# Performance work log

Hardware: AMD Instinct MI355X
Metric: run time of the kernel (lower is better)

The kernel has to match this reference:

```python
import jax, jax.numpy as jnp
import numpy as np

H = 5120       # hidden_size
NH = 128       # num_heads
QLR = 1536     # q_lora_rank
DR = 64        # qk_rope_head_dim
KVLR = 512     # kv_lora_rank
DV = 128       # v_head_dim
DN = 128       # qk_nope_head_dim
DQ = 192       # q_head_dim
THETA = 10000.0
EPS = 1e-6


def _rmsnorm(x, w, eps=EPS):
    xf = x.astype(jnp.float32)
    var = jnp.mean(xf * xf, axis=-1, keepdims=True)
    return (w * (xf * jax.lax.rsqrt(var + eps))).astype(x.dtype)


def _rope(x, cos, sin):
    # Llama-style complex rotation on interleaved pairs along last dim.
    xr = x.reshape(x.shape[:-1] + (-1, 2))
    x0, x1 = xr[..., 0], xr[..., 1]
    out = jnp.stack([x0 * cos - x1 * sin, x0 * sin + x1 * cos], axis=-1)
    return out.reshape(x.shape)


def setup_inputs() -> dict:
    key = jax.random.key(0)
    ks = jax.random.split(key, 8)
    b, kv_len = 2, 2048
    s = 0.02  # scaled-down normal init for numerical sanity (math unchanged)
    return {
        "hidden_states": jax.random.normal(ks[0], (b, 1, H), jnp.float32),
        "compressed_kv_normed_cache": jax.random.normal(ks[1], (b, kv_len, KVLR), jnp.float32),
        "k_pe_cache": jax.random.normal(ks[2], (b, kv_len, DR), jnp.float32),
        "q_a_w": jax.random.normal(ks[3], (QLR, H), jnp.float32) * s,
        "q_a_ln_w": jnp.ones((QLR,), jnp.float32),
        "q_b_w": jax.random.normal(ks[4], (NH * DQ, QLR), jnp.float32) * s,
        "kv_b_w": jax.random.normal(ks[5], (NH * (DN + DV), KVLR), jnp.float32) * s,
        "o_w": jax.random.normal(ks[6], (H, NH * DV), jnp.float32) * s,
    }


def reference(hidden_states, compressed_kv_normed_cache, k_pe_cache,
              q_a_w, q_a_ln_w, q_b_w, kv_b_w, o_w):
    b = hidden_states.shape[0]
    kv_len = k_pe_cache.shape[1]

    # Q path: down-proj -> RMSNorm -> up-proj
    q_a = jnp.einsum('bqh,rh->bqr', hidden_states, q_a_w)          # [b,1,QLR]
    q_a = _rmsnorm(q_a, q_a_ln_w)
    q = jnp.einsum('bqr,or->bqo', q_a, q_b_w).reshape(b, NH, DQ)   # q_len==1
    q_nope, q_pe = q[..., :DN], q[..., DN:]                        # [b,NH,128],[b,NH,64]

    # RoPE tables
    inv_freq = 1.0 / (THETA ** (jnp.arange(0, DR, 2, dtype=jnp.float32) / DR))  # [32]
    ang = jnp.arange(kv_len, dtype=jnp.float32)[:, None] * inv_freq             # [kv_len,32]
    cos, sin = jnp.cos(ang), jnp.sin(ang)

    # query rotated at position kv_len-1 (torch code repeats q then takes last slot)
    q_pe = _rope(q_pe, cos[-1], sin[-1])                           # [b,NH,64]
    k_pe = _rope(k_pe_cache, cos[None], sin[None])                 # [b,kv_len,64]

    # KV decompression (shared latent -> per-head nope-key and value)
    kv = jnp.einsum('bkc,oc->bko', compressed_kv_normed_cache, kv_b_w)
    kv = kv.reshape(b, kv_len, NH, DN + DV)
    k_nope, v = kv[..., :DN], kv[..., DN:]                         # [b,kv,NH,128] each

    # scores: nope part + rope part (k_pe broadcast across heads)
    scores = (jnp.einsum('bhd,bkhd->bhk', q_nope, k_nope)
              + jnp.einsum('bhd,bkd->bhk', q_pe, k_pe)) * (DQ ** -0.5)
    attn = jax.nn.softmax(scores.astype(jnp.float32), axis=-1).astype(hidden_states.dtype)

    out = jnp.einsum('bhk,bkhd->bhd', attn, v).reshape(b, 1, NH * DV)
    return jnp.einsum('bqo,ho->bqh', out, o_w)                     # [b,1,H]
```

## Files before the change

### kernel.cpp

```cpp
#include <hip/hip_runtime.h>
#include <math.h>

constexpr int kH    = 5120;
constexpr int kQLR  = 1536;
constexpr int kNH   = 128;
constexpr int kDQ   = 192;
constexpr int kDN   = 128;
constexpr int kDR   = 64;
constexpr int kKVLR = 512;
constexpr int kDV   = 128;

template<int IN, int SPLIT, bool ATOMIC>
__global__ __launch_bounds__(256) void gemv2_k(const float* __restrict__ W,
                                               const float* __restrict__ x,
                                               float* __restrict__ y, int R) {
  constexpr int CH = IN / SPLIT;
  constexpr int F4 = CH / 256;
  int lane = threadIdx.x & 63, wave = threadIdx.x >> 6;
  int r0 = blockIdx.x * 8 + wave * 2;
  int c0 = blockIdx.y * CH;
  const float4* W0 = (const float4*)(W + (size_t)r0 * IN + c0);
  const float4* W1 = (const float4*)(W + (size_t)(r0 + 1) * IN + c0);
  const float4* x0 = (const float4*)(x + c0);
  const float4* x1 = (const float4*)(x + IN + c0);
  float a00 = 0.f, a01 = 0.f, a10 = 0.f, a11 = 0.f;
#pragma unroll 4
  for (int i = 0; i < F4; ++i) {
    int idx = lane + (i << 6);
    float4 w0 = W0[idx];
    float4 w1 = W1[idx];
    float4 u = x0[idx];
    float4 v = x1[idx];
    a00 = fmaf(w0.x,u.x,fmaf(w0.y,u.y,fmaf(w0.z,u.z,fmaf(w0.w,u.w,a00))));
    a01 = fmaf(w0.x,v.x,fmaf(w0.y,v.y,fmaf(w0.z,v.z,fmaf(w0.w,v.w,a01))));
    a10 = fmaf(w1.x,u.x,fmaf(w1.y,u.y,fmaf(w1.z,u.z,fmaf(w1.w,u.w,a10))));
    a11 = fmaf(w1.x,v.x,fmaf(w1.y,v.y,fmaf(w1.z,v.z,fmaf(w1.w,v.w,a11))));
  }
#pragma unroll
  for (int off = 32; off > 0; off >>= 1) {
    a00 += __shfl_down(a00, off, 64);
    a01 += __shfl_down(a01, off, 64);
    a10 += __shfl_down(a10, off, 64);
    a11 += __shfl_down(a11, off, 64);
  }
  if (lane == 0) {
    if (ATOMIC) {
      atomicAdd(&y[r0], a00);
      atomicAdd(&y[(size_t)R + r0], a01);
      atomicAdd(&y[r0 + 1], a10);
      atomicAdd(&y[(size_t)R + r0 + 1], a11);
    } else {
      y[r0] = a00;
      y[(size_t)R + r0] = a01;
      y[r0 + 1] = a10;
      y[(size_t)R + r0 + 1] = a11;
    }
  }
}

__global__ __launch_bounds__(256) void rmsnorm_k(const float* __restrict__ qa,
                                                 const float* __restrict__ w,
                                                 float* __restrict__ out) {
  int b = blockIdx.x, t = threadIdx.x;
  const float* x = qa + (size_t)b * kQLR;
  float s = 0.f;
  for (int i = t; i < kQLR; i += 256) { float v = x[i]; s = fmaf(v, v, s); }
  __shared__ float red[4];
#pragma unroll
  for (int off = 32; off > 0; off >>= 1) s += __shfl_down(s, off, 64);
  if ((t & 63) == 0) red[t >> 6] = s;
  __syncthreads();
  float tot = red[0] + red[1] + red[2] + red[3];
  float scale = rsqrtf(tot / (float)kQLR + 1e-6f);
  for (int i = t; i < kQLR; i += 256) out[(size_t)b * kQLR + i] = x[i] * scale * w[i];
}

__global__ __launch_bounds__(256) void rope_q_k(float* __restrict__ q, int pos) {
  int p = blockIdx.x * 256 + threadIdx.x;
  int i = p & 31;
  int h = (p >> 5) & (kNH - 1);
  int b = p >> 12;
  float inv = powf(10000.0f, -(float)i * (1.0f / 32.0f));
  float ang = (float)pos * inv;
  float s, c;
  sincosf(ang, &s, &c);
  float* base = q + ((size_t)b * kNH + h) * kDQ + kDN + 2 * i;
  float x0 = base[0], x1 = base[1];
  base[0] = x0 * c - x1 * s;
  base[1] = x0 * s + x1 * c;
}

__global__ __launch_bounds__(256) void rope_k_k(const float* __restrict__ kin,
                                                float* __restrict__ kout, int KV) {
  int p = blockIdx.x * 256 + threadIdx.x;
  int i = p & 31;
  int bk = p >> 5;
  int b = bk / KV;
  int k = bk - b * KV;
  float inv = powf(10000.0f, -(float)i * (1.0f / 32.0f));
  float ang = (float)k * inv;
  float s, c;
  sincosf(ang, &s, &c);
  const float* src = kin + ((size_t)b * KV + k) * kDR + 2 * i;
  float* dst = kout + ((size_t)b * KV + k) * kDR + 2 * i;
  float x0 = src[0], x1 = src[1];
  dst[0] = x0 * c - x1 * s;
  dst[1] = x0 * s + x1 * c;
}

__global__ __launch_bounds__(256) void qabs_k(const float* __restrict__ q,
                                              const float* __restrict__ kvw,
                                              float* __restrict__ qabs) {
  int h = blockIdx.x, ds = blockIdx.y;
  int t = threadIdx.x;
  __shared__ float qn[2][32];
  if (t < 64) {
    int b = t >> 5, d = t & 31;
    qn[b][d] = q[((size_t)b * kNH + h) * kDQ + ds * 32 + d];
  }
  __syncthreads();
  float a0x = 0.f, a0y = 0.f, a1x = 0.f, a1y = 0.f;
  const float* wb = kvw + ((size_t)h * 256 + ds * 32) * kKVLR + t * 2;
#pragma unroll 4
  for (int d = 0; d < 32; ++d) {
    float2 w = *(const float2*)(wb + (size_t)d * kKVLR);
    float q0 = qn[0][d], q1 = qn[1][d];
    a0x = fmaf(q0, w.x, a0x); a0y = fmaf(q0, w.y, a0y);
    a1x = fmaf(q1, w.x, a1x); a1y = fmaf(q1, w.y, a1y);
  }
  float* p0 = qabs + (size_t)h * kKVLR + t * 2;
  float* p1 = qabs + ((size_t)kNH + h) * kKVLR + t * 2;
  atomicAdd(p0, a0x); atomicAdd(p0 + 1, a0y);
  atomicAdd(p1, a1x); atomicAdd(p1 + 1, a1y);
}

__global__ __launch_bounds__(256) void scores_k(const float* __restrict__ qabs,
                                                const float* __restrict__ qfull,
                                                const float* __restrict__ c,
                                                const float* __restrict__ kper,
                                                float* __restrict__ scores, int KV) {
  int kc = blockIdx.x, hg = blockIdx.y, b = blockIdx.z;
  int t = threadIdx.x, lane = t & 63, wave = t >> 6;
  int h0 = __builtin_amdgcn_readfirstlane(hg * 16 + wave * 4);
  int k0 = kc * 64;
  __shared__ float cl[64 * 129];
  __shared__ float kl[64 * 65];
  float acc[4] = {0.f, 0.f, 0.f, 0.f};

  {
    const float4* src = (const float4*)(kper + ((size_t)b * KV + k0) * kDR);
#pragma unroll
    for (int i = 0; i < 4; ++i) {
      int idx = t + i * 256;
      int r = idx >> 4, c4 = idx & 15;
      float4 v = src[r * 16 + c4];
      float* d = &kl[r * 65 + (c4 << 2)];
      d[0] = v.x; d[1] = v.y; d[2] = v.z; d[3] = v.w;
    }
  }

  for (int cch = 0; cch < 4; ++cch) {
    __syncthreads();
    const float* cb = c + ((size_t)b * KV + k0) * kKVLR + cch * 128;
#pragma unroll
    for (int i = 0; i < 8; ++i) {
      int idx = t + i * 256;
      int r = idx >> 5, c4 = idx & 31;
      float4 v = *(const float4*)(cb + (size_t)r * kKVLR + (c4 << 2));
      float* d = &cl[r * 129 + (c4 << 2)];
      d[0] = v.x; d[1] = v.y; d[2] = v.z; d[3] = v.w;
    }
    __syncthreads();
    const float* qb = qabs + ((size_t)b * kNH + h0) * kKVLR + cch * 128;
#pragma unroll 4
    for (int cc = 0; cc < 128; ++cc) {
      float cv = cl[lane * 129 + cc];
#pragma unroll
      for (int j = 0; j < 4; ++j)
        acc[j] = fmaf(cv, qb[(size_t)j * kKVLR + cc], acc[j]);
    }
  }

  {
    const float* qp = qfull + ((size_t)b * kNH + h0) * kDQ + kDN;
#pragma unroll 4
    for (int i = 0; i < 64; ++i) {
      float kv = kl[lane * 65 + i];
#pragma unroll
      for (int j = 0; j < 4; ++j)
        acc[j] = fmaf(kv, qp[j * kDQ + i], acc[j]);
    }
  }

  const float scale = 1.0f / sqrtf(192.0f);
#pragma unroll
  for (int j = 0; j < 4; ++j)
    scores[((size_t)b * kNH + h0 + j) * KV + k0 + lane] = acc[j] * scale;
}

__global__ __launch_bounds__(256) void softmax_k(float* __restrict__ sc, int KV) {
  int t = threadIdx.x;
  float* row = sc + (size_t)blockIdx.x * KV;
  float vals[8];
  float m = -1e30f;
#pragma unroll
  for (int i = 0; i < 8; ++i) {
    vals[i] = row[t + i * 256];
    m = fmaxf(m, vals[i]);
  }
  __shared__ float red[4];
#pragma unroll
  for (int off = 32; off > 0; off >>= 1) m = fmaxf(m, __shfl_down(m, off, 64));
  if ((t & 63) == 0) red[t >> 6] = m;
  __syncthreads();
  m = fmaxf(fmaxf(red[0], red[1]), fmaxf(red[2], red[3]));
  __syncthreads();
  float s = 0.f;
#pragma unroll
  for (int i = 0; i < 8; ++i) {
    vals[i] = __expf(vals[i] - m);
    s += vals[i];
  }
#pragma unroll
  for (int off = 32; off > 0; off >>= 1) s += __shfl_down(s, off, 64);
  if ((t & 63) == 0) red[t >> 6] = s;
  __syncthreads();
  s = red[0] + red[1] + red[2] + red[3];
  float inv = 1.0f / s;
#pragma unroll
  for (int i = 0; i < 8; ++i) row[t + i * 256] = vals[i] * inv;
}

__global__ __launch_bounds__(256) void ctx_partial_k(const float* __restrict__ attn,
                                                     const float* __restrict__ c,
                                                     float* __restrict__ ctxp, int KV) {
  int ks = blockIdx.x, hg = blockIdx.y, b = blockIdx.z;
  int t = threadIdx.x;
  int k0 = ks * 64, h0 = hg * 16;
  __shared__ float al[64 * 20];
#pragma unroll
  for (int i = 0; i < 4; ++i) {
    int idx = t + i * 256;
    int j = idx >> 6, k = idx & 63;
    al[k * 20 + j] = attn[((size_t)b * kNH + h0 + j) * KV + k0 + k];
  }
  __syncthreads();
  float2 acc[16];
#pragma unroll
  for (int j = 0; j < 16; ++j) acc[j] = make_float2(0.f, 0.f);
  const float2* c2 = (const float2*)(c + ((size_t)b * KV + k0) * kKVLR);
#pragma unroll 2
  for (int k = 0; k < 64; ++k) {
    float2 cv = c2[k * (kKVLR / 2) + t];
#pragma unroll
    for (int j4 = 0; j4 < 4; ++j4) {
      float4 av = *(const float4*)&al[k * 20 + j4 * 4];
      acc[j4*4+0].x = fmaf(av.x, cv.x, acc[j4*4+0].x);
      acc[j4*4+0].y = fmaf(av.x, cv.y, acc[j4*4+0].y);
      acc[j4*4+1].x = fmaf(av.y, cv.x, acc[j4*4+1].x);
      acc[j4*4+1].y = fmaf(av.y, cv.y, acc[j4*4+1].y);
      acc[j4*4+2].x = fmaf(av.z, cv.x, acc[j4*4+2].x);
      acc[j4*4+2].y = fmaf(av.z, cv.y, acc[j4*4+2].y);
      acc[j4*4+3].x = fmaf(av.w, cv.x, acc[j4*4+3].x);
      acc[j4*4+3].y = fmaf(av.w, cv.y, acc[j4*4+3].y);
    }
  }
#pragma unroll
  for (int j = 0; j < 16; ++j) {
    float2* dst = (float2*)(ctxp + (((size_t)ks * 2 + b) * kNH + h0 + j) * kKVLR);
    dst[t] = acc[j];
  }
}

__global__ __launch_bounds__(256) void vproj_k(const float* __restrict__ ctxp,
                                               const float* __restrict__ kvw,
                                               float* __restrict__ oh) {
  int h = blockIdx.x, dq = blockIdx.y;
  int t = threadIdx.x, lane = t & 63, wave = t >> 6;
  __shared__ float cf[2 * kKVLR];
  {
    int b = t >> 7, g = t & 127;
    float4 s = make_float4(0.f, 0.f, 0.f, 0.f);
#pragma unroll 8
    for (int ks = 0; ks < 32; ++ks) {
      const float4* p = (const float4*)(ctxp + (((size_t)ks * 2 + b) * kNH + h) * kKVLR);
      float4 v = p[g];
      s.x += v.x; s.y += v.y; s.z += v.z; s.w += v.w;
    }
    *(float4*)&cf[b * kKVLR + (g << 2)] = s;
  }
  __syncthreads();
  float cr0[8], cr1[8];
#pragma unroll
  for (int j = 0; j < 8; ++j) {
    cr0[j] = cf[lane * 8 + j];
    cr1[j] = cf[kKVLR + lane * 8 + j];
  }
#pragma unroll
  for (int i = 0; i < 8; ++i) {
    int d = dq * 32 + wave * 8 + i;
    const float4* w4 = (const float4*)(kvw + ((size_t)h * 256 + 128 + d) * kKVLR) + lane * 2;
    float4 wa = w4[0], wb = w4[1];
    float s0 = wa.x * cr0[0] + wa.y * cr0[1] + wa.z * cr0[2] + wa.w * cr0[3]
             + wb.x * cr0[4] + wb.y * cr0[5] + wb.z * cr0[6] + wb.w * cr0[7];
    float s1 = wa.x * cr1[0] + wa.y * cr1[1] + wa.z * cr1[2] + wa.w * cr1[3]
             + wb.x * cr1[4] + wb.y * cr1[5] + wb.z * cr1[6] + wb.w * cr1[7];
#pragma unroll
    for (int off = 32; off > 0; off >>= 1) {
      s0 += __shfl_down(s0, off, 64);
      s1 += __shfl_down(s1, off, 64);
    }
    if (lane == 0) {
      oh[(size_t)h * kDV + d] = s0;
      oh[((size_t)kNH + h) * kDV + d] = s1;
    }
  }
}

extern "C" void kernel_launch(void* const* d_in, const int* in_sizes, int n_in,
                              void* d_out, int out_size, void* d_ws, size_t ws_size,
                              hipStream_t stream) {
  const float* hs   = (const float*)d_in[0];
  const float* ckv  = (const float*)d_in[1];
  const float* kpe  = (const float*)d_in[2];
  const float* qaw  = (const float*)d_in[3];
  const float* qlnw = (const float*)d_in[4];
  const float* qbw  = (const float*)d_in[5];
  const float* kvbw = (const float*)d_in[6];
  const float* ow   = (const float*)d_in[7];
  float* out = (float*)d_out;

  int B  = in_sizes[0] / kH;
  int KV = in_sizes[2] / (B * kDR);

  float* ws   = (float*)d_ws;
  float* qa   = ws;
  float* qan  = qa + 4096;
  float* q    = qan + 4096;
  float* qabs = q + (size_t)B * kNH * kDQ;
  float* kper = qabs + (size_t)B * kNH * kKVLR;
  float* sc   = kper + (size_t)B * KV * kDR;
  float* ctxp = sc + (size_t)B * kNH * KV;
  float* oh   = ctxp + (size_t)32 * B * kNH * kKVLR;

  hipMemsetAsync(qa, 0, (size_t)B * kQLR * sizeof(float), stream);
  hipMemsetAsync(qabs, 0, (size_t)B * kNH * kKVLR * sizeof(float), stream);
  hipMemsetAsync(out, 0, (size_t)out_size * sizeof(float), stream);

  gemv2_k<kH, 4, true><<<dim3(kQLR / 8, 4), 256, 0, stream>>>(qaw, hs, qa, kQLR);
  rmsnorm_k<<<B, 256, 0, stream>>>(qa, qlnw, qan);
  gemv2_k<kQLR, 1, false><<<dim3((kNH * kDQ) / 8, 1), 256, 0, stream>>>(qbw, qan, q, kNH * kDQ);
  rope_q_k<<<(B * kNH * 32) / 256, 256, 0, stream>>>(q, KV - 1);
  rope_k_k<<<(B * KV * 32) / 256, 256, 0, stream>>>(kpe, kper, KV);
  qabs_k<<<dim3(kNH, 4), 256, 0, stream>>>(q, kvbw, qabs);
  scores_k<<<dim3(KV / 64, 8, B), 256, 0, stream>>>(qabs, q, ckv, kper, sc, KV);
  softmax_k<<<B * kNH, 256, 0, stream>>>(sc, KV);
  ctx_partial_k<<<dim3(32, 8, B), 256, 0, stream>>>(sc, ckv, ctxp, KV);
  vproj_k<<<dim3(kNH, 4), 256, 0, stream>>>(ctxp, kvbw, oh);
  gemv2_k<kNH * kDV, 4, true><<<dim3(kH / 8, 4), 256, 0, stream>>>(ow, oh, out, kH);
}
```

Baseline: 669.5 us.

## Fuse RoPE, scores, softmax and context into split-softmax attention kernel

Replaces the separate RoPE, score, softmax and context-partial kernels with one kernel per 64-key chunk. It applies RoPE to keys and the query on the fly, computes a local softmax (max and sum) per head and chunk, and accumulates unnormalized context partials. The v-projection kernel then rescales and merges the 32 chunk partials using the stored max/sum pairs and divides by the global normalizer. This removes four launches and the global score round trip, at the cost of recomputing sincos per block and adding rescale work in the merge.

```diff
diff --git a/kernel.cpp b/kernel.cpp
--- a/kernel.cpp
+++ b/kernel.cpp
@@ -75,39 +75,6 @@
   for (int i = t; i < kQLR; i += 256) out[(size_t)b * kQLR + i] = x[i] * scale * w[i];
 }
 
-__global__ __launch_bounds__(256) void rope_q_k(float* __restrict__ q, int pos) {
-  int p = blockIdx.x * 256 + threadIdx.x;
-  int i = p & 31;
-  int h = (p >> 5) & (kNH - 1);
-  int b = p >> 12;
-  float inv = powf(10000.0f, -(float)i * (1.0f / 32.0f));
-  float ang = (float)pos * inv;
-  float s, c;
-  sincosf(ang, &s, &c);
-  float* base = q + ((size_t)b * kNH + h) * kDQ + kDN + 2 * i;
-  float x0 = base[0], x1 = base[1];
-  base[0] = x0 * c - x1 * s;
-  base[1] = x0 * s + x1 * c;
-}
-
-__global__ __launch_bounds__(256) void rope_k_k(const float* __restrict__ kin,
-                                                float* __restrict__ kout, int KV) {
-  int p = blockIdx.x * 256 + threadIdx.x;
-  int i = p & 31;
-  int bk = p >> 5;
-  int b = bk / KV;
-  int k = bk - b * KV;
-  float inv = powf(10000.0f, -(float)i * (1.0f / 32.0f));
-  float ang = (float)k * inv;
-  float s, c;
-  sincosf(ang, &s, &c);
-  const float* src = kin + ((size_t)b * KV + k) * kDR + 2 * i;
-  float* dst = kout + ((size_t)b * KV + k) * kDR + 2 * i;
-  float x0 = src[0], x1 = src[1];
-  dst[0] = x0 * c - x1 * s;
-  dst[1] = x0 * s + x1 * c;
-}
-
 __global__ __launch_bounds__(256) void qabs_k(const float* __restrict__ q,
                                               const float* __restrict__ kvw,
                                               float* __restrict__ qabs) {
@@ -134,31 +101,58 @@
   atomicAdd(p1, a1x); atomicAdd(p1 + 1, a1y);
 }
 
-__global__ __launch_bounds__(256) void scores_k(const float* __restrict__ qabs,
-                                                const float* __restrict__ qfull,
-                                                const float* __restrict__ c,
-                                                const float* __restrict__ kper,
-                                                float* __restrict__ scores, int KV) {
-  int kc = blockIdx.x, hg = blockIdx.y, b = blockIdx.z;
+__global__ __launch_bounds__(256) void attn_k(const float* __restrict__ qabs,
+                                              const float* __restrict__ qfull,
+                                              const float* __restrict__ c,
+                                              const float* __restrict__ kpe,
+                                              float* __restrict__ ctxp,
+                                              float* __restrict__ ml, int KV) {
+  int ks = blockIdx.x, hg = blockIdx.y, b = blockIdx.z;
   int t = threadIdx.x, lane = t & 63, wave = t >> 6;
   int h0 = __builtin_amdgcn_readfirstlane(hg * 16 + wave * 4);
-  int k0 = kc * 64;
+  int k0 = ks * 64;
   __shared__ float cl[64 * 129];
   __shared__ float kl[64 * 65];
-  float acc[4] = {0.f, 0.f, 0.f, 0.f};
+  __shared__ float ql[16 * 64];
+  __shared__ float al[64 * 20];
+
+  constexpr float kNegLog = -0.28782313662425572f;
 
   {
-    const float4* src = (const float4*)(kper + ((size_t)b * KV + k0) * kDR);
+    const float4* src = (const float4*)(kpe + ((size_t)b * KV + k0) * kDR);
 #pragma unroll
     for (int i = 0; i < 4; ++i) {
       int idx = t + i * 256;
       int r = idx >> 4, c4 = idx & 15;
       float4 v = src[r * 16 + c4];
+      float fk = (float)(k0 + r);
+      float inv0 = expf(kNegLog * (float)(c4 * 2));
+      float inv1 = expf(kNegLog * (float)(c4 * 2 + 1));
+      float s0, c0, s1, c1;
+      sincosf(fk * inv0, &s0, &c0);
+      sincosf(fk * inv1, &s1, &c1);
       float* d = &kl[r * 65 + (c4 << 2)];
-      d[0] = v.x; d[1] = v.y; d[2] = v.z; d[3] = v.w;
-    }
-  }
-
+      d[0] = v.x * c0 - v.y * s0;
+      d[1] = v.x * s0 + v.y * c0;
+      d[2] = v.z * c1 - v.w * s1;
+      d[3] = v.z * s1 + v.w * c1;
+    }
+  }
+  {
+    float fp = (float)(KV - 1);
+    for (int pi = t; pi < 512; pi += 256) {
+      int j = pi >> 5, i = pi & 31;
+      float inv = expf(kNegLog * (float)i);
+      float s, cc;
+      sincosf(fp * inv, &s, &cc);
+      const float* qp = qfull + ((size_t)b * kNH + hg * 16 + j) * kDQ + kDN + 2 * i;
+      float x0 = qp[0], x1 = qp[1];
+      ql[j * 64 + 2 * i]     = x0 * cc - x1 * s;
+      ql[j * 64 + 2 * i + 1] = x0 * s + x1 * cc;
+    }
+  }
+
+  float acc[4] = {0.f, 0.f, 0.f, 0.f};
   for (int cch = 0; cch < 4; ++cch) {
     __syncthreads();
     const float* cb = c + ((size_t)b * KV + k0) * kKVLR + cch * 128;
@@ -173,81 +167,50 @@
     __syncthreads();
     const float* qb = qabs + ((size_t)b * kNH + h0) * kKVLR + cch * 128;
 #pragma unroll 4
-    for (int cc = 0; cc < 128; ++cc) {
-      float cv = cl[lane * 129 + cc];
+    for (int cc2 = 0; cc2 < 128; ++cc2) {
+      float cv = cl[lane * 129 + cc2];
 #pragma unroll
       for (int j = 0; j < 4; ++j)
-        acc[j] = fmaf(cv, qb[(size_t)j * kKVLR + cc], acc[j]);
-    }
-  }
-
+        acc[j] = fmaf(cv, qb[(size_t)j * kKVLR + cc2], acc[j]);
+    }
+  }
   {
-    const float* qp = qfull + ((size_t)b * kNH + h0) * kDQ + kDN;
 #pragma unroll 4
     for (int i = 0; i < 64; ++i) {
       float kv = kl[lane * 65 + i];
 #pragma unroll
       for (int j = 0; j < 4; ++j)
-        acc[j] = fmaf(kv, qp[j * kDQ + i], acc[j]);
+        acc[j] = fmaf(kv, ql[(wave * 4 + j) * 64 + i], acc[j]);
     }
   }
 
   const float scale = 1.0f / sqrtf(192.0f);
-#pragma unroll
-  for (int j = 0; j < 4; ++j)
-    scores[((size_t)b * kNH + h0 + j) * KV + k0 + lane] = acc[j] * scale;
-}
-
-__global__ __launch_bounds__(256) void softmax_k(float* __restrict__ sc, int KV) {
-  int t = threadIdx.x;
-  float* row = sc + (size_t)blockIdx.x * KV;
-  float vals[8];
-  float m = -1e30f;
-#pragma unroll
-  for (int i = 0; i < 8; ++i) {
-    vals[i] = row[t + i * 256];
-    m = fmaxf(m, vals[i]);
-  }
-  __shared__ float red[4];
-#pragma unroll
-  for (int off = 32; off > 0; off >>= 1) m = fmaxf(m, __shfl_down(m, off, 64));
-  if ((t & 63) == 0) red[t >> 6] = m;
+  float pj[4], mj[4], lj[4];
+#pragma unroll
+  for (int j = 0; j < 4; ++j) {
+    float s = acc[j] * scale;
+    float m = s;
+#pragma unroll
+    for (int off = 32; off > 0; off >>= 1) m = fmaxf(m, __shfl_xor(m, off, 64));
+    float p = __expf(s - m);
+    float l = p;
+#pragma unroll
+    for (int off = 32; off > 0; off >>= 1) l += __shfl_xor(l, off, 64);
+    pj[j] = p; mj[j] = m; lj[j] = l;
+  }
+  *(float4*)&al[lane * 20 + wave * 4] = make_float4(pj[0], pj[1], pj[2], pj[3]);
+  if (lane == 0) {
+#pragma unroll
+    for (int j = 0; j < 4; ++j) {
+      float2* mp = (float2*)(ml + (((size_t)b * kNH + h0 + j) * 32 + ks) * 2);
+      *mp = make_float2(mj[j], lj[j]);
+    }
+  }
   __syncthreads();
-  m = fmaxf(fmaxf(red[0], red[1]), fmaxf(red[2], red[3]));
-  __syncthreads();
-  float s = 0.f;
-#pragma unroll
-  for (int i = 0; i < 8; ++i) {
-    vals[i] = __expf(vals[i] - m);
-    s += vals[i];
-  }
-#pragma unroll
-  for (int off = 32; off > 0; off >>= 1) s += __shfl_down(s, off, 64);
-  if ((t & 63) == 0) red[t >> 6] = s;
-  __syncthreads();
-  s = red[0] + red[1] + red[2] + red[3];
-  float inv = 1.0f / s;
-#pragma unroll
-  for (int i = 0; i < 8; ++i) row[t + i * 256] = vals[i] * inv;
-}
-
-__global__ __launch_bounds__(256) void ctx_partial_k(const float* __restrict__ attn,
-                                                     const float* __restrict__ c,
-                                                     float* __restrict__ ctxp, int KV) {
-  int ks = blockIdx.x, hg = blockIdx.y, b = blockIdx.z;
-  int t = threadIdx.x;
-  int k0 = ks * 64, h0 = hg * 16;
-  __shared__ float al[64 * 20];
-#pragma unroll
-  for (int i = 0; i < 4; ++i) {
-    int idx = t + i * 256;
-    int j = idx >> 6, k = idx & 63;
-    al[k * 20 + j] = attn[((size_t)b * kNH + h0 + j) * KV + k0 + k];
-  }
-  __syncthreads();
-  float2 acc[16];
-#pragma unroll
-  for (int j = 0; j < 16; ++j) acc[j] = make_float2(0.f, 0.f);
+
+  float2 accv[16];
+#pragma unroll
+  for (int j = 0; j < 16; ++j) accv[j] = make_float2(0.f, 0.f);
   const float2* c2 = (const float2*)(c + ((size_t)b * KV + k0) * kKVLR);
 #pragma unroll 2
   for (int k = 0; k < 64; ++k) {
@@ -255,39 +218,53 @@
 #pragma unroll
     for (int j4 = 0; j4 < 4; ++j4) {
       float4 av = *(const float4*)&al[k * 20 + j4 * 4];
-      acc[j4*4+0].x = fmaf(av.x, cv.x, acc[j4*4+0].x);
-      acc[j4*4+0].y = fmaf(av.x, cv.y, acc[j4*4+0].y);
-      acc[j4*4+1].x = fmaf(av.y, cv.x, acc[j4*4+1].x);
-      acc[j4*4+1].y = fmaf(av.y, cv.y, acc[j4*4+1].y);
-      acc[j4*4+2].x = fmaf(av.z, cv.x, acc[j4*4+2].x);
-      acc[j4*4+2].y = fmaf(av.z, cv.y, acc[j4*4+2].y);
-      acc[j4*4+3].x = fmaf(av.w, cv.x, acc[j4*4+3].x);
-      acc[j4*4+3].y = fmaf(av.w, cv.y, acc[j4*4+3].y);
+      accv[j4*4+0].x = fmaf(av.x, cv.x, accv[j4*4+0].x);
+      accv[j4*4+0].y = fmaf(av.x, cv.y, accv[j4*4+0].y);
+      accv[j4*4+1].x = fmaf(av.y, cv.x, accv[j4*4+1].x);
+      accv[j4*4+1].y = fmaf(av.y, cv.y, accv[j4*4+1].y);
+      accv[j4*4+2].x = fmaf(av.z, cv.x, accv[j4*4+2].x);
+      accv[j4*4+2].y = fmaf(av.z, cv.y, accv[j4*4+2].y);
+      accv[j4*4+3].x = fmaf(av.w, cv.x, accv[j4*4+3].x);
+      accv[j4*4+3].y = fmaf(av.w, cv.y, accv[j4*4+3].y);
     }
   }
 #pragma unroll
   for (int j = 0; j < 16; ++j) {
-    float2* dst = (float2*)(ctxp + (((size_t)ks * 2 + b) * kNH + h0 + j) * kKVLR);
-    dst[t] = acc[j];
+    float2* dst = (float2*)(ctxp + (((size_t)ks * 2 + b) * kNH + hg * 16 + j) * kKVLR);
+    dst[t] = accv[j];
   }
 }
 
 __global__ __launch_bounds__(256) void vproj_k(const float* __restrict__ ctxp,
+                                               const float* __restrict__ ml,
                                                const float* __restrict__ kvw,
                                                float* __restrict__ oh) {
   int h = blockIdx.x, dq = blockIdx.y;
   int t = threadIdx.x, lane = t & 63, wave = t >> 6;
   __shared__ float cf[2 * kKVLR];
+  __shared__ float invl[2];
   {
     int b = t >> 7, g = t & 127;
-    float4 s = make_float4(0.f, 0.f, 0.f, 0.f);
+    const float2* mlb = (const float2*)(ml + ((size_t)b * kNH + h) * 64);
+    float M = -1e30f;
 #pragma unroll 8
-    for (int ks = 0; ks < 32; ++ks) {
-      const float4* p = (const float4*)(ctxp + (((size_t)ks * 2 + b) * kNH + h) * kKVLR);
+    for (int s = 0; s < 32; ++s) M = fmaxf(M, mlb[s].x);
+    float L = 0.f;
+    float4 a4 = make_float4(0.f, 0.f, 0.f, 0.f);
+#pragma unroll 4
+    for (int s = 0; s < 32; ++s) {
+      float2 e = mlb[s];
+      float w = __expf(e.x - M);
+      L = fmaf(w, e.y, L);
+      const float4* p = (const float4*)(ctxp + (((size_t)s * 2 + b) * kNH + h) * kKVLR);
       float4 v = p[g];
-      s.x += v.x; s.y += v.y; s.z += v.z; s.w += v.w;
-    }
-    *(float4*)&cf[b * kKVLR + (g << 2)] = s;
+      a4.x = fmaf(w, v.x, a4.x);
+      a4.y = fmaf(w, v.y, a4.y);
+      a4.z = fmaf(w, v.z, a4.z);
+      a4.w = fmaf(w, v.w, a4.w);
+    }
+    *(float4*)&cf[b * kKVLR + (g << 2)] = a4;
+    if (g == 0) invl[b] = 1.0f / L;
   }
   __syncthreads();
   float cr0[8], cr1[8];
@@ -311,8 +288,8 @@
       s1 += __shfl_down(s1, off, 64);
     }
     if (lane == 0) {
-      oh[(size_t)h * kDV + d] = s0;
-      oh[((size_t)kNH + h) * kDV + d] = s1;
+      oh[(size_t)h * kDV + d] = s0 * invl[0];
+      oh[((size_t)kNH + h) * kDV + d] = s1 * invl[1];
     }
   }
 }
@@ -335,27 +312,21 @@
 
   float* ws   = (float*)d_ws;
   float* qa   = ws;
-  float* qan  = qa + 4096;
-  float* q    = qan + 4096;
-  float* qabs = q + (size_t)B * kNH * kDQ;
-  float* kper = qabs + (size_t)B * kNH * kKVLR;
-  float* sc   = kper + (size_t)B * KV * kDR;
-  float* ctxp = sc + (size_t)B * kNH * KV;
-  float* oh   = ctxp + (size_t)32 * B * kNH * kKVLR;
-
-  hipMemsetAsync(qa, 0, (size_t)B * kQLR * sizeof(float), stream);
-  hipMemsetAsync(qabs, 0, (size_t)B * kNH * kKVLR * sizeof(float), stream);
+  float* qabs = qa + (size_t)B * kQLR;
+  float* qan  = qabs + (size_t)B * kNH * kKVLR;
+  float* q    = qan + (size_t)B * kQLR;
+  float* ctxp = q + (size_t)B * kNH * kDQ;
+  float* ml   = ctxp + (size_t)32 * B * kNH * kKVLR;
+  float* oh   = ml + (size_t)B * kNH * 64;
+
+  hipMemsetAsync(qa, 0, ((size_t)B * kQLR + (size_t)B * kNH * kKVLR) * sizeof(float), stream);
   hipMemsetAsync(out, 0, (size_t)out_size * sizeof(float), stream);
 
   gemv2_k<kH, 4, true><<<dim3(kQLR / 8, 4), 256, 0, stream>>>(qaw, hs, qa, kQLR);
   rmsnorm_k<<<B, 256, 0, stream>>>(qa, qlnw, qan);
   gemv2_k<kQLR, 1, false><<<dim3((kNH * kDQ) / 8, 1), 256, 0, stream>>>(qbw, qan, q, kNH * kDQ);
-  rope_q_k<<<(B * kNH * 32) / 256, 256, 0, stream>>>(q, KV - 1);
-  rope_k_k<<<(B * KV * 32) / 256, 256, 0, stream>>>(kpe, kper, KV);
   qabs_k<<<dim3(kNH, 4), 256, 0, stream>>>(q, kvbw, qabs);
-  scores_k<<<dim3(KV / 64, 8, B), 256, 0, stream>>>(qabs, q, ckv, kper, sc, KV);
-  softmax_k<<<B * kNH, 256, 0, stream>>>(sc, KV);
-  ctx_partial_k<<<dim3(32, 8, B), 256, 0, stream>>>(sc, ckv, ctxp, KV);
-  vproj_k<<<dim3(kNH, 4), 256, 0, stream>>>(ctxp, kvbw, oh);
+  attn_k<<<dim3(KV / 64, 8, B), 256, 0, stream>>>(qabs, q, ckv, kpe, ctxp, ml, KV);
+  vproj_k<<<dim3(kNH, 4), 256, 0, stream>>>(ctxp, ml, kvbw, oh);
   gemv2_k<kNH * kDV, 4, true><<<dim3(kH / 8, 4), 256, 0, stream>>>(ow, oh, out, kH);
 }
```

Result: no change. 662.0 us (-1.1%).
